# Performance work log

Hardware: AMD Instinct MI355X
Metric: run time of the kernel (lower is better)

Reference implementation:

```python
import jax, jax.numpy as jnp
import numpy as np

DIM = 224
HEADS = 8
DH = 28
WS = 8
INNER = DH * HEADS  # 224
SCALE = DH ** -0.5
B, H, W = 256, 32, 32


def setup_inputs() -> dict:
    key = jax.random.key(0)
    ks = jax.random.split(key, 6)
    x = jax.random.normal(ks[0], (B, H, W, DIM), jnp.float32)
    Wq = jax.random.normal(ks[1], (DIM, INNER), jnp.float32) * 0.02
    Wkv = jax.random.normal(ks[2], (DIM, 2 * INNER), jnp.float32) * 0.02
    Wo = jax.random.normal(ks[3], (INNER, DIM), jnp.float32) * 0.02
    bo = jnp.zeros((DIM,), jnp.float32)
    seq_l1 = WS * WS                      # 64 tokens per window
    hw = 256 // HEADS                     # 32
    seq_l2 = hw * hw // seq_l1            # 16 windows
    pos_emb1 = jax.random.normal(ks[4], (1, 1, HEADS // 2, seq_l1, seq_l1), jnp.float32)
    pos_emb2 = jax.random.normal(ks[5], (1, 1, HEADS // 2, seq_l2, seq_l2), jnp.float32)
    return {"x": x, "Wq": Wq, "Wkv": Wkv, "Wo": Wo, "bo": bo,
            "pos_emb1": pos_emb1, "pos_emb2": pos_emb2}


def _win_part(t):
    # [b, H, W, c] -> [b, n_windows, WS*WS, c]
    b, h, w, c = t.shape
    t = t.reshape(b, h // WS, WS, w // WS, WS, c).transpose(0, 1, 3, 2, 4, 5)
    return t.reshape(b, (h // WS) * (w // WS), WS * WS, c)


def _win_merge(t, h, w):
    # [b, n_windows, WS*WS, c] -> [b, H, W, c]
    b, n, mm, c = t.shape
    t = t.reshape(b, h // WS, w // WS, WS, WS, c).transpose(0, 1, 3, 2, 4, 5)
    return t.reshape(b, h, w, c)


def _attn(q, k, v, pos):
    # q,k,v: [b, n, mm, ch]; split into HEADS//2 heads of dim d
    b, n, mm, ch = q.shape
    hh = HEADS // 2
    d = ch // hh
    def sp(t):
        return t.reshape(b, n, mm, hh, d).transpose(0, 1, 3, 2, 4)  # [b,n,hh,mm,d]
    q, k, v = sp(q) * SCALE, sp(k), sp(v)
    sim = jnp.einsum('bnhid,bnhjd->bnhij', q, k) + pos
    sim = jnp.roll(sim, (1, 1), axis=(3, 4))
    attn = jax.nn.softmax(sim, axis=-1)
    o = jnp.einsum('bnhij,bnhjd->bnhid', attn, v)
    return o.transpose(0, 1, 3, 2, 4).reshape(b, n, mm, ch)


def reference(x, Wq, Wkv, Wo, bo, pos_emb1, pos_emb2):
    b, h, w, c = x.shape
    q = x @ Wq
    kv = x @ Wkv
    k, v = kv[..., :INNER], kv[..., INNER:]
    half = c // 2
    # Branch 1: local attention within each 8x8 window (first half of channels)
    q1, k1, v1 = (_win_part(t[..., :half]) for t in (q, k, v))
    out1 = _attn(q1, k1, v1, pos_emb1)  # [b, n, mm, half]
    # Branch 2: attention across windows at same intra-window position (second half)
    q2, k2, v2 = (_win_part(t[..., half:]).transpose(0, 2, 1, 3) for t in (q, k, v))
    out2 = _attn(q2, k2, v2, pos_emb2).transpose(0, 2, 1, 3)  # [b, n, mm, half]
    out = jnp.concatenate([out1, out2], axis=-1) @ Wo + bo
    return _win_merge(out, h, w)
```

## Files before the change

### kernel.cpp

```cpp
#include <hip/hip_runtime.h>

typedef __bf16 bf16_t;
typedef __bf16 bf16x4 __attribute__((ext_vector_type(4)));
typedef __bf16 bf16x8 __attribute__((ext_vector_type(8)));
typedef float  f32x4  __attribute__((ext_vector_type(4)));

#define MFMA16(a, b, c) __builtin_amdgcn_mfma_f32_16x16x32_bf16((a), (b), (c), 0, 0, 0)

#define ATT_SCALE 0.1889822365046136f

__device__ __forceinline__ bf16x8 load8_masked(const bf16_t* p, bool full) {
  bf16x4 lo = *reinterpret_cast<const bf16x4*>(p);
  bf16x4 hi = {};
  if (full) hi = *reinterpret_cast<const bf16x4*>(p + 4);
  bf16x8 r;
  r[0] = lo[0]; r[1] = lo[1]; r[2] = lo[2]; r[3] = lo[3];
  r[4] = hi[0]; r[5] = hi[1]; r[6] = hi[2]; r[7] = hi[3];
  return r;
}

__global__ __launch_bounds__(256) void prep_w(
    const float* __restrict__ Wq, const float* __restrict__ Wkv,
    const float* __restrict__ Wo,
    bf16_t* __restrict__ wsw_qkv, bf16_t* __restrict__ wsw_o) {
  const int id = blockIdx.x * 256 + threadIdx.x;
  const int buf = id / 6272;
  const int rem = id % 6272;
  const int ks = rem / 896, rem2 = rem % 896;
  const int nt = rem2 / 64, lane = rem2 % 64;
  const int col = lane & 15, g = lane >> 4;
  const int n = nt * 16 + col;
  const int k0 = ks * 32 + g * 8;
  const float* src;
  int stride;
  if (buf == 0)      { src = Wq + n;        stride = 224; }
  else if (buf == 1) { src = Wkv + n;       stride = 448; }
  else if (buf == 2) { src = Wkv + 224 + n; stride = 448; }
  else               { src = Wo + n;        stride = 224; }
  bf16x8 o;
#pragma unroll
  for (int e = 0; e < 8; ++e) o[e] = (bf16_t)src[(size_t)(k0 + e) * stride];
  bf16_t* dst = (buf < 3) ? (wsw_qkv + buf * 100352) : wsw_o;
  *reinterpret_cast<bf16x8*>(dst + ((ks * 14 + nt) * 64 + lane) * 8) = o;
}

__global__ __launch_bounds__(256, 4) void qkv_gemm(
    const float* __restrict__ x, const bf16_t* __restrict__ wsw,
    bf16_t* __restrict__ q, bf16_t* __restrict__ k, bf16_t* __restrict__ v) {
  __shared__ bf16_t xs[64][232];
  const int tid = threadIdx.x;
  const int blk = blockIdx.x;
  const int mt = blk / 3, chunk = blk % 3;
  const int b = mt >> 4, win = mt & 15;
  for (int idx = tid; idx < 64 * 56; idx += 256) {
    const int r = idx / 56, c4 = idx % 56;
    const int hh = ((win >> 2) << 3) | (r >> 3);
    const int ww = ((win & 3) << 3) | (r & 7);
    const float4 f = *reinterpret_cast<const float4*>(
        x + (size_t)((b * 32 + hh) * 32 + ww) * 224 + c4 * 4);
    bf16x4 o;
    o[0] = (bf16_t)f.x; o[1] = (bf16_t)f.y; o[2] = (bf16_t)f.z; o[3] = (bf16_t)f.w;
    *reinterpret_cast<bf16x4*>(&xs[r][c4 * 4]) = o;
  }
  const int lane = tid & 63, wid = tid >> 6;
  const int col = lane & 15, g = lane >> 4;
  const int wr = wid >> 1, wc = wid & 1;
  const bf16_t* wt = wsw + chunk * 100352;
  bf16_t* dst = (chunk == 0) ? q : ((chunk == 1) ? k : v);
  f32x4 acc[2][7];
  const f32x4 vzero = {0.f, 0.f, 0.f, 0.f};
#pragma unroll
  for (int ti = 0; ti < 2; ++ti)
#pragma unroll
    for (int tj = 0; tj < 7; ++tj) acc[ti][tj] = vzero;
  __syncthreads();
#pragma unroll
  for (int ks = 0; ks < 7; ++ks) {
    bf16x8 af0 = *reinterpret_cast<const bf16x8*>(&xs[wr * 32 + col][ks * 32 + g * 8]);
    bf16x8 af1 = *reinterpret_cast<const bf16x8*>(&xs[wr * 32 + 16 + col][ks * 32 + g * 8]);
#pragma unroll
    for (int tj = 0; tj < 7; ++tj) {
      const bf16x8 bfr = *reinterpret_cast<const bf16x8*>(
          wt + (((ks * 14) + wc * 7 + tj) * 64 + lane) * 8);
      acc[0][tj] = MFMA16(af0, bfr, acc[0][tj]);
      acc[1][tj] = MFMA16(af1, bfr, acc[1][tj]);
    }
  }
  const size_t base = (size_t)mt * 64;
#pragma unroll
  for (int ti = 0; ti < 2; ++ti)
#pragma unroll
    for (int tj = 0; tj < 7; ++tj)
#pragma unroll
      for (int r = 0; r < 4; ++r) {
        const int row = wr * 32 + ti * 16 + g * 4 + r;
        const int cn = wc * 112 + tj * 16 + col;
        dst[(base + row) * 224 + cn] = (bf16_t)acc[ti][tj][r];
      }
}

__global__ __launch_bounds__(256) void attn1(
    const bf16_t* __restrict__ q, const bf16_t* __restrict__ k,
    const bf16_t* __restrict__ v, const float* __restrict__ pos1,
    bf16_t* __restrict__ ao) {
  __shared__ bf16_t Vt[4][32][72];
  __shared__ bf16_t Pl[4][64][72];
  const int tid = threadIdx.x, blk = blockIdx.x;
  const int wid = tid >> 6, lane = tid & 63;
  const int col = lane & 15, g = lane >> 4;
  const size_t rowbase = (size_t)blk * 64;
  {
    const bf16_t* src = v + (rowbase + lane) * 224 + 28 * wid;
    const int j = (lane + 63) & 63;
#pragma unroll
    for (int c = 0; c < 28; c += 4) {
      const bf16x4 d = *reinterpret_cast<const bf16x4*>(src + c);
      Vt[wid][c + 0][j] = d[0]; Vt[wid][c + 1][j] = d[1];
      Vt[wid][c + 2][j] = d[2]; Vt[wid][c + 3][j] = d[3];
    }
#pragma unroll
    for (int c = 28; c < 32; ++c) Vt[wid][c][lane] = (bf16_t)0.f;
  }
  bf16x8 aQ[4], bK[4];
#pragma unroll
  for (int t = 0; t < 4; ++t) {
    const size_t off = (rowbase + t * 16 + col) * 224 + 28 * wid + 8 * g;
    aQ[t] = load8_masked(q + off, g < 3);
    bK[t] = load8_masked(k + off, g < 3);
  }
  const f32x4 vzero = {0.f, 0.f, 0.f, 0.f};
  f32x4 s[4][4];
#pragma unroll
  for (int ti = 0; ti < 4; ++ti)
#pragma unroll
    for (int tj = 0; tj < 4; ++tj)
      s[ti][tj] = MFMA16(aQ[ti], bK[tj], vzero);
  const float* pe = pos1 + wid * 4096;
#pragma unroll
  for (int ti = 0; ti < 4; ++ti)
#pragma unroll
    for (int tj = 0; tj < 4; ++tj)
#pragma unroll
      for (int r = 0; r < 4; ++r)
        s[ti][tj][r] = s[ti][tj][r] * ATT_SCALE +
                       pe[(ti * 16 + g * 4 + r) * 64 + tj * 16 + col];
#pragma unroll
  for (int ti = 0; ti < 4; ++ti) {
#pragma unroll
    for (int r = 0; r < 4; ++r) {
      float m = fmaxf(fmaxf(s[ti][0][r], s[ti][1][r]), fmaxf(s[ti][2][r], s[ti][3][r]));
#pragma unroll
      for (int d = 1; d < 16; d <<= 1) m = fmaxf(m, __shfl_xor(m, d));
      float sum = 0.f;
#pragma unroll
      for (int tj = 0; tj < 4; ++tj) {
        const float e = __expf(s[ti][tj][r] - m);
        s[ti][tj][r] = e; sum += e;
      }
#pragma unroll
      for (int d = 1; d < 16; d <<= 1) sum += __shfl_xor(sum, d);
      const float inv = 1.f / sum;
#pragma unroll
      for (int tj = 0; tj < 4; ++tj) s[ti][tj][r] *= inv;
    }
  }
#pragma unroll
  for (int ti = 0; ti < 4; ++ti)
#pragma unroll
    for (int tj = 0; tj < 4; ++tj)
#pragma unroll
      for (int r = 0; r < 4; ++r)
        Pl[wid][ti * 16 + g * 4 + r][tj * 16 + col] = (bf16_t)s[ti][tj][r];
  __syncthreads();
#pragma unroll
  for (int ti = 0; ti < 4; ++ti)
#pragma unroll
    for (int t2 = 0; t2 < 2; ++t2) {
      f32x4 o = vzero;
#pragma unroll
      for (int ks = 0; ks < 2; ++ks) {
        const bf16x8 aP = *reinterpret_cast<const bf16x8*>(&Pl[wid][ti * 16 + col][ks * 32 + g * 8]);
        const bf16x8 bV = *reinterpret_cast<const bf16x8*>(&Vt[wid][t2 * 16 + col][ks * 32 + g * 8]);
        o = MFMA16(aP, bV, o);
      }
      const int ch = t2 * 16 + col;
      if (ch < 28) {
#pragma unroll
        for (int r = 0; r < 4; ++r) {
          const int i = ti * 16 + g * 4 + r;
          ao[(rowbase + ((i + 1) & 63)) * 224 + 28 * wid + ch] = (bf16_t)o[r];
        }
      }
    }
}

__global__ __launch_bounds__(256) void attn2(
    const bf16_t* __restrict__ q, const bf16_t* __restrict__ k,
    const bf16_t* __restrict__ v, const float* __restrict__ pos2,
    bf16_t* __restrict__ ao) {
  __shared__ bf16_t Vt2[4][32][40];
  __shared__ bf16_t P2[4][16][40];
  const int tid = threadIdx.x, blk = blockIdx.x;
  const int wid = tid >> 6, lane = tid & 63;
  const int col = lane & 15, g = lane >> 4;
  const int b = blk >> 4;
  const int pos = (blk & 15) * 4 + wid;
  {
    unsigned short* z1 = reinterpret_cast<unsigned short*>(&Vt2[wid][0][0]);
    for (int i = lane; i < 32 * 40; i += 64) z1[i] = 0;
    unsigned short* z2 = reinterpret_cast<unsigned short*>(&P2[wid][0][0]);
    for (int i = lane; i < 16 * 40; i += 64) z2[i] = 0;
  }
  __syncthreads();
  const f32x4 vzero = {0.f, 0.f, 0.f, 0.f};
  for (int h = 0; h < 4; ++h) {
    {
      const bf16_t* src = v + ((size_t)(b * 16 + col) * 64 + pos) * 224 + 112 + 28 * h + 7 * g;
      const int jd = (col + 15) & 15;
#pragma unroll
      for (int i = 0; i < 7; ++i) Vt2[wid][7 * g + i][jd] = src[i];
    }
    const size_t off = ((size_t)(b * 16 + col) * 64 + pos) * 224 + 112 + 28 * h + 8 * g;
    const bf16x8 aQ = load8_masked(q + off, g < 3);
    const bf16x8 bK = load8_masked(k + off, g < 3);
    f32x4 s = MFMA16(aQ, bK, vzero);
    const float* pe = pos2 + h * 256;
#pragma unroll
    for (int r = 0; r < 4; ++r)
      s[r] = s[r] * ATT_SCALE + pe[(g * 4 + r) * 16 + col];
#pragma unroll
    for (int r = 0; r < 4; ++r) {
      float m = s[r];
#pragma unroll
      for (int d = 1; d < 16; d <<= 1) m = fmaxf(m, __shfl_xor(m, d));
      const float e = __expf(s[r] - m);
      float sum = e;
#pragma unroll
      for (int d = 1; d < 16; d <<= 1) sum += __shfl_xor(sum, d);
      s[r] = e / sum;
    }
#pragma unroll
    for (int r = 0; r < 4; ++r) P2[wid][g * 4 + r][col] = (bf16_t)s[r];
    __syncthreads();
    const bf16x8 aP = *reinterpret_cast<const bf16x8*>(&P2[wid][col][g * 8]);
#pragma unroll
    for (int t2 = 0; t2 < 2; ++t2) {
      const bf16x8 bV = *reinterpret_cast<const bf16x8*>(&Vt2[wid][t2 * 16 + col][g * 8]);
      const f32x4 o = MFMA16(aP, bV, vzero);
      const int ch = t2 * 16 + col;
      if (ch < 28) {
#pragma unroll
        for (int r = 0; r < 4; ++r) {
          const int wo = ((g * 4 + r) + 1) & 15;
          ao[((size_t)(b * 16 + wo) * 64 + pos) * 224 + 112 + 28 * h + ch] = (bf16_t)o[r];
        }
      }
    }
    __syncthreads();
  }
}

__global__ __launch_bounds__(256, 4) void out_gemm(
    const bf16_t* __restrict__ ao, const bf16_t* __restrict__ wsw,
    const float* __restrict__ bo, float* __restrict__ out) {
  __shared__ bf16_t xs[64][232];
  const int tid = threadIdx.x, blk = blockIdx.x;
  for (int idx = tid; idx < 64 * 28; idx += 256) {
    const int r = idx / 28, sg = idx % 28;
    *reinterpret_cast<uint4*>(&xs[r][sg * 8]) =
        *reinterpret_cast<const uint4*>(ao + ((size_t)blk * 64 + r) * 224 + sg * 8);
  }
  const int lane = tid & 63, wid = tid >> 6;
  const int col = lane & 15, g = lane >> 4;
  const int wr = wid >> 1, wc = wid & 1;
  f32x4 acc[2][7];
  const f32x4 vzero = {0.f, 0.f, 0.f, 0.f};
#pragma unroll
  for (int ti = 0; ti < 2; ++ti)
#pragma unroll
    for (int tj = 0; tj < 7; ++tj) acc[ti][tj] = vzero;
  __syncthreads();
#pragma unroll
  for (int ks = 0; ks < 7; ++ks) {
    bf16x8 af0 = *reinterpret_cast<const bf16x8*>(&xs[wr * 32 + col][ks * 32 + g * 8]);
    bf16x8 af1 = *reinterpret_cast<const bf16x8*>(&xs[wr * 32 + 16 + col][ks * 32 + g * 8]);
#pragma unroll
    for (int tj = 0; tj < 7; ++tj) {
      const bf16x8 bfr = *reinterpret_cast<const bf16x8*>(
          wsw + (((ks * 14) + wc * 7 + tj) * 64 + lane) * 8);
      acc[0][tj] = MFMA16(af0, bfr, acc[0][tj]);
      acc[1][tj] = MFMA16(af1, bfr, acc[1][tj]);
    }
  }
  float bias[7];
#pragma unroll
  for (int tj = 0; tj < 7; ++tj) bias[tj] = bo[wc * 112 + tj * 16 + col];
  const int b = blk >> 4, win = blk & 15;
#pragma unroll
  for (int ti = 0; ti < 2; ++ti)
#pragma unroll
    for (int tj = 0; tj < 7; ++tj)
#pragma unroll
      for (int r = 0; r < 4; ++r) {
        const int p = wr * 32 + ti * 16 + g * 4 + r;
        const int cn = wc * 112 + tj * 16 + col;
        const int hh = ((win >> 2) << 3) | (p >> 3);
        const int ww = ((win & 3) << 3) | (p & 7);
        out[(size_t)((b * 32 + hh) * 32 + ww) * 224 + cn] = acc[ti][tj][r] + bias[tj];
      }
}

extern "C" void kernel_launch(void* const* d_in, const int* in_sizes, int n_in,
                              void* d_out, int out_size, void* d_ws, size_t ws_size,
                              hipStream_t stream) {
  const float* x   = (const float*)d_in[0];
  const float* Wq  = (const float*)d_in[1];
  const float* Wkv = (const float*)d_in[2];
  const float* Wo  = (const float*)d_in[3];
  const float* bo  = (const float*)d_in[4];
  const float* p1  = (const float*)d_in[5];
  const float* p2  = (const float*)d_in[6];
  char* w = (char*)d_ws;
  bf16_t* q_ws    = (bf16_t*)(w);
  bf16_t* k_ws    = (bf16_t*)(w + 117440512);
  bf16_t* v_ws    = (bf16_t*)(w + 234881024);
  bf16_t* ao_ws   = (bf16_t*)(w + 352321536);
  bf16_t* wsw_qkv = (bf16_t*)(w + 469762048);
  bf16_t* wsw_o   = (bf16_t*)(w + 470063104);

  prep_w<<<98, 256, 0, stream>>>(Wq, Wkv, Wo, wsw_qkv, wsw_o);
  qkv_gemm<<<12288, 256, 0, stream>>>(x, wsw_qkv, q_ws, k_ws, v_ws);
  attn1<<<4096, 256, 0, stream>>>(q_ws, k_ws, v_ws, p1, ao_ws);
  attn2<<<4096, 256, 0, stream>>>(q_ws, k_ws, v_ws, p2, ao_ws);
  out_gemm<<<4096, 256, 0, stream>>>(ao_ws, wsw_o, bo, (float*)d_out);
}
```

Baseline: 1.010 ms.

## Fuse QKV chunks per block, split Q/K/V by branch with branch-2 transposed layout

Each qkv_gemm block now computes all three Q/K/V chunks from one staged x tile instead of three blocks each re-reading and converting x. It writes branch-1 and branch-2 halves into separate 112-wide buffers, with branch 2 stored window-transposed so attn2 reads contiguous rows instead of strided gathers. attn1 moves to 512 threads, splitting query rows across two wave groups per head. The cost is fewer qkv blocks with a serial chunk loop and a larger workspace.

```diff
diff --git a/kernel.cpp b/kernel.cpp
--- a/kernel.cpp
+++ b/kernel.cpp
@@ -46,11 +46,10 @@
 
 __global__ __launch_bounds__(256, 4) void qkv_gemm(
     const float* __restrict__ x, const bf16_t* __restrict__ wsw,
-    bf16_t* __restrict__ q, bf16_t* __restrict__ k, bf16_t* __restrict__ v) {
+    bf16_t* __restrict__ q1, bf16_t* __restrict__ k1, bf16_t* __restrict__ v1,
+    bf16_t* __restrict__ q2, bf16_t* __restrict__ k2, bf16_t* __restrict__ v2) {
   __shared__ bf16_t xs[64][232];
-  const int tid = threadIdx.x;
-  const int blk = blockIdx.x;
-  const int mt = blk / 3, chunk = blk % 3;
+  const int tid = threadIdx.x, mt = blockIdx.x;
   const int b = mt >> 4, win = mt & 15;
   for (int idx = tid; idx < 64 * 56; idx += 256) {
     const int r = idx / 56, c4 = idx % 56;
@@ -65,41 +64,57 @@
   const int lane = tid & 63, wid = tid >> 6;
   const int col = lane & 15, g = lane >> 4;
   const int wr = wid >> 1, wc = wid & 1;
-  const bf16_t* wt = wsw + chunk * 100352;
-  bf16_t* dst = (chunk == 0) ? q : ((chunk == 1) ? k : v);
-  f32x4 acc[2][7];
   const f32x4 vzero = {0.f, 0.f, 0.f, 0.f};
-#pragma unroll
-  for (int ti = 0; ti < 2; ++ti)
-#pragma unroll
-    for (int tj = 0; tj < 7; ++tj) acc[ti][tj] = vzero;
   __syncthreads();
-#pragma unroll
-  for (int ks = 0; ks < 7; ++ks) {
-    bf16x8 af0 = *reinterpret_cast<const bf16x8*>(&xs[wr * 32 + col][ks * 32 + g * 8]);
-    bf16x8 af1 = *reinterpret_cast<const bf16x8*>(&xs[wr * 32 + 16 + col][ks * 32 + g * 8]);
-#pragma unroll
-    for (int tj = 0; tj < 7; ++tj) {
-      const bf16x8 bfr = *reinterpret_cast<const bf16x8*>(
-          wt + (((ks * 14) + wc * 7 + tj) * 64 + lane) * 8);
-      acc[0][tj] = MFMA16(af0, bfr, acc[0][tj]);
-      acc[1][tj] = MFMA16(af1, bfr, acc[1][tj]);
-    }
-  }
-  const size_t base = (size_t)mt * 64;
-#pragma unroll
-  for (int ti = 0; ti < 2; ++ti)
-#pragma unroll
-    for (int tj = 0; tj < 7; ++tj)
-#pragma unroll
-      for (int r = 0; r < 4; ++r) {
-        const int row = wr * 32 + ti * 16 + g * 4 + r;
-        const int cn = wc * 112 + tj * 16 + col;
-        dst[(base + row) * 224 + cn] = (bf16_t)acc[ti][tj][r];
-      }
-}
-
-__global__ __launch_bounds__(256) void attn1(
+#pragma unroll 1
+  for (int chunk = 0; chunk < 3; ++chunk) {
+    const bf16_t* wt = wsw + chunk * 100352;
+    f32x4 acc[2][7];
+#pragma unroll
+    for (int ti = 0; ti < 2; ++ti)
+#pragma unroll
+      for (int tj = 0; tj < 7; ++tj) acc[ti][tj] = vzero;
+#pragma unroll
+    for (int ks = 0; ks < 7; ++ks) {
+      bf16x8 af0 = *reinterpret_cast<const bf16x8*>(&xs[wr * 32 + col][ks * 32 + g * 8]);
+      bf16x8 af1 = *reinterpret_cast<const bf16x8*>(&xs[wr * 32 + 16 + col][ks * 32 + g * 8]);
+#pragma unroll
+      for (int tj = 0; tj < 7; ++tj) {
+        const bf16x8 bfr = *reinterpret_cast<const bf16x8*>(
+            wt + (((ks * 14) + wc * 7 + tj) * 64 + lane) * 8);
+        acc[0][tj] = MFMA16(af0, bfr, acc[0][tj]);
+        acc[1][tj] = MFMA16(af1, bfr, acc[1][tj]);
+      }
+    }
+    bf16_t* d1 = (chunk == 0) ? q1 : ((chunk == 1) ? k1 : v1);
+    bf16_t* d2 = (chunk == 0) ? q2 : ((chunk == 1) ? k2 : v2);
+    if (wc == 0) {
+#pragma unroll
+      for (int ti = 0; ti < 2; ++ti)
+#pragma unroll
+        for (int tj = 0; tj < 7; ++tj)
+#pragma unroll
+          for (int r = 0; r < 4; ++r) {
+            const int row = wr * 32 + ti * 16 + g * 4 + r;
+            const int cn = tj * 16 + col;
+            d1[((size_t)mt * 64 + row) * 112 + cn] = (bf16_t)acc[ti][tj][r];
+          }
+    } else {
+#pragma unroll
+      for (int ti = 0; ti < 2; ++ti)
+#pragma unroll
+        for (int tj = 0; tj < 7; ++tj)
+#pragma unroll
+          for (int r = 0; r < 4; ++r) {
+            const int row = wr * 32 + ti * 16 + g * 4 + r;
+            const int cn = tj * 16 + col;
+            d2[(((size_t)b * 64 + row) * 16 + win) * 112 + cn] = (bf16_t)acc[ti][tj][r];
+          }
+    }
+  }
+}
+
+__global__ __launch_bounds__(512) void attn1(
     const bf16_t* __restrict__ q, const bf16_t* __restrict__ k,
     const bf16_t* __restrict__ v, const float* __restrict__ pos1,
     bf16_t* __restrict__ ao) {
@@ -107,45 +122,50 @@
   __shared__ bf16_t Pl[4][64][72];
   const int tid = threadIdx.x, blk = blockIdx.x;
   const int wid = tid >> 6, lane = tid & 63;
+  const int head = wid & 3, rh = wid >> 2;
   const int col = lane & 15, g = lane >> 4;
   const size_t rowbase = (size_t)blk * 64;
-  {
-    const bf16_t* src = v + (rowbase + lane) * 224 + 28 * wid;
+  if (rh == 0) {
+    const bf16_t* src = v + (rowbase + lane) * 112 + 28 * head;
     const int j = (lane + 63) & 63;
 #pragma unroll
     for (int c = 0; c < 28; c += 4) {
       const bf16x4 d = *reinterpret_cast<const bf16x4*>(src + c);
-      Vt[wid][c + 0][j] = d[0]; Vt[wid][c + 1][j] = d[1];
-      Vt[wid][c + 2][j] = d[2]; Vt[wid][c + 3][j] = d[3];
-    }
-#pragma unroll
-    for (int c = 28; c < 32; ++c) Vt[wid][c][lane] = (bf16_t)0.f;
-  }
-  bf16x8 aQ[4], bK[4];
+      Vt[head][c + 0][j] = d[0]; Vt[head][c + 1][j] = d[1];
+      Vt[head][c + 2][j] = d[2]; Vt[head][c + 3][j] = d[3];
+    }
+#pragma unroll
+    for (int c = 28; c < 32; ++c) Vt[head][c][lane] = (bf16_t)0.f;
+  }
+  bf16x8 aQ[2], bK[4];
+#pragma unroll
+  for (int t = 0; t < 2; ++t) {
+    const size_t off = (rowbase + (rh * 2 + t) * 16 + col) * 112 + 28 * head + 8 * g;
+    aQ[t] = load8_masked(q + off, g < 3);
+  }
 #pragma unroll
   for (int t = 0; t < 4; ++t) {
-    const size_t off = (rowbase + t * 16 + col) * 224 + 28 * wid + 8 * g;
-    aQ[t] = load8_masked(q + off, g < 3);
+    const size_t off = (rowbase + t * 16 + col) * 112 + 28 * head + 8 * g;
     bK[t] = load8_masked(k + off, g < 3);
   }
   const f32x4 vzero = {0.f, 0.f, 0.f, 0.f};
-  f32x4 s[4][4];
-#pragma unroll
-  for (int ti = 0; ti < 4; ++ti)
+  f32x4 s[2][4];
+#pragma unroll
+  for (int ti = 0; ti < 2; ++ti)
 #pragma unroll
     for (int tj = 0; tj < 4; ++tj)
       s[ti][tj] = MFMA16(aQ[ti], bK[tj], vzero);
-  const float* pe = pos1 + wid * 4096;
-#pragma unroll
-  for (int ti = 0; ti < 4; ++ti)
+  const float* pe = pos1 + head * 4096;
+#pragma unroll
+  for (int ti = 0; ti < 2; ++ti)
 #pragma unroll
     for (int tj = 0; tj < 4; ++tj)
 #pragma unroll
       for (int r = 0; r < 4; ++r)
         s[ti][tj][r] = s[ti][tj][r] * ATT_SCALE +
-                       pe[(ti * 16 + g * 4 + r) * 64 + tj * 16 + col];
-#pragma unroll
-  for (int ti = 0; ti < 4; ++ti) {
+                       pe[((rh * 2 + ti) * 16 + g * 4 + r) * 64 + tj * 16 + col];
+#pragma unroll
+  for (int ti = 0; ti < 2; ++ti) {
 #pragma unroll
     for (int r = 0; r < 4; ++r) {
       float m = fmaxf(fmaxf(s[ti][0][r], s[ti][1][r]), fmaxf(s[ti][2][r], s[ti][3][r]));
@@ -165,38 +185,40 @@
     }
   }
 #pragma unroll
-  for (int ti = 0; ti < 4; ++ti)
+  for (int ti = 0; ti < 2; ++ti)
 #pragma unroll
     for (int tj = 0; tj < 4; ++tj)
 #pragma unroll
       for (int r = 0; r < 4; ++r)
-        Pl[wid][ti * 16 + g * 4 + r][tj * 16 + col] = (bf16_t)s[ti][tj][r];
+        Pl[head][(rh * 2 + ti) * 16 + g * 4 + r][tj * 16 + col] = (bf16_t)s[ti][tj][r];
   __syncthreads();
 #pragma unroll
-  for (int ti = 0; ti < 4; ++ti)
+  for (int ti = 0; ti < 2; ++ti)
 #pragma unroll
     for (int t2 = 0; t2 < 2; ++t2) {
       f32x4 o = vzero;
 #pragma unroll
       for (int ks = 0; ks < 2; ++ks) {
-        const bf16x8 aP = *reinterpret_cast<const bf16x8*>(&Pl[wid][ti * 16 + col][ks * 32 + g * 8]);
-        const bf16x8 bV = *reinterpret_cast<const bf16x8*>(&Vt[wid][t2 * 16 + col][ks * 32 + g * 8]);
+        const bf16x8 aP = *reinterpret_cast<const bf16x8*>(
+            &Pl[head][(rh * 2 + ti) * 16 + col][ks * 32 + g * 8]);
+        const bf16x8 bV = *reinterpret_cast<const bf16x8*>(
+            &Vt[head][t2 * 16 + col][ks * 32 + g * 8]);
         o = MFMA16(aP, bV, o);
       }
       const int ch = t2 * 16 + col;
       if (ch < 28) {
 #pragma unroll
         for (int r = 0; r < 4; ++r) {
-          const int i = ti * 16 + g * 4 + r;
-          ao[(rowbase + ((i + 1) & 63)) * 224 + 28 * wid + ch] = (bf16_t)o[r];
+          const int i = (rh * 2 + ti) * 16 + g * 4 + r;
+          ao[(rowbase + ((i + 1) & 63)) * 224 + 28 * head + ch] = (bf16_t)o[r];
         }
       }
     }
 }
 
 __global__ __launch_bounds__(256) void attn2(
-    const bf16_t* __restrict__ q, const bf16_t* __restrict__ k,
-    const bf16_t* __restrict__ v, const float* __restrict__ pos2,
+    const bf16_t* __restrict__ q2, const bf16_t* __restrict__ k2,
+    const bf16_t* __restrict__ v2, const float* __restrict__ pos2,
     bf16_t* __restrict__ ao) {
   __shared__ bf16_t Vt2[4][32][40];
   __shared__ bf16_t P2[4][16][40];
@@ -205,6 +227,7 @@
   const int col = lane & 15, g = lane >> 4;
   const int b = blk >> 4;
   const int pos = (blk & 15) * 4 + wid;
+  const size_t base = ((size_t)b * 64 + pos) * 16;
   {
     unsigned short* z1 = reinterpret_cast<unsigned short*>(&Vt2[wid][0][0]);
     for (int i = lane; i < 32 * 40; i += 64) z1[i] = 0;
@@ -215,14 +238,14 @@
   const f32x4 vzero = {0.f, 0.f, 0.f, 0.f};
   for (int h = 0; h < 4; ++h) {
     {
-      const bf16_t* src = v + ((size_t)(b * 16 + col) * 64 + pos) * 224 + 112 + 28 * h + 7 * g;
+      const bf16_t* src = v2 + (base + col) * 112 + 28 * h + 7 * g;
       const int jd = (col + 15) & 15;
 #pragma unroll
       for (int i = 0; i < 7; ++i) Vt2[wid][7 * g + i][jd] = src[i];
     }
-    const size_t off = ((size_t)(b * 16 + col) * 64 + pos) * 224 + 112 + 28 * h + 8 * g;
-    const bf16x8 aQ = load8_masked(q + off, g < 3);
-    const bf16x8 bK = load8_masked(k + off, g < 3);
+    const size_t off = (base + col) * 112 + 28 * h + 8 * g;
+    const bf16x8 aQ = load8_masked(q2 + off, g < 3);
+    const bf16x8 bK = load8_masked(k2 + off, g < 3);
     f32x4 s = MFMA16(aQ, bK, vzero);
     const float* pe = pos2 + h * 256;
 #pragma unroll
@@ -321,16 +344,21 @@
   const float* p1  = (const float*)d_in[5];
   const float* p2  = (const float*)d_in[6];
   char* w = (char*)d_ws;
-  bf16_t* q_ws    = (bf16_t*)(w);
-  bf16_t* k_ws    = (bf16_t*)(w + 117440512);
-  bf16_t* v_ws    = (bf16_t*)(w + 234881024);
-  bf16_t* ao_ws   = (bf16_t*)(w + 352321536);
-  bf16_t* wsw_qkv = (bf16_t*)(w + 469762048);
-  bf16_t* wsw_o   = (bf16_t*)(w + 470063104);
+  const size_t HSZ = 58720256;
+  bf16_t* q1_ws   = (bf16_t*)(w);
+  bf16_t* k1_ws   = (bf16_t*)(w + HSZ);
+  bf16_t* v1_ws   = (bf16_t*)(w + 2 * HSZ);
+  bf16_t* q2_ws   = (bf16_t*)(w + 3 * HSZ);
+  bf16_t* k2_ws   = (bf16_t*)(w + 4 * HSZ);
+  bf16_t* v2_ws   = (bf16_t*)(w + 5 * HSZ);
+  bf16_t* ao_ws   = (bf16_t*)(w + 6 * HSZ);
+  bf16_t* wsw_qkv = (bf16_t*)(w + 6 * HSZ + 117440512);
+  bf16_t* wsw_o   = (bf16_t*)(w + 6 * HSZ + 117440512 + 602112);
 
   prep_w<<<98, 256, 0, stream>>>(Wq, Wkv, Wo, wsw_qkv, wsw_o);
-  qkv_gemm<<<12288, 256, 0, stream>>>(x, wsw_qkv, q_ws, k_ws, v_ws);
-  attn1<<<4096, 256, 0, stream>>>(q_ws, k_ws, v_ws, p1, ao_ws);
-  attn2<<<4096, 256, 0, stream>>>(q_ws, k_ws, v_ws, p2, ao_ws);
+  qkv_gemm<<<4096, 256, 0, stream>>>(x, wsw_qkv, q1_ws, k1_ws, v1_ws,
+                                     q2_ws, k2_ws, v2_ws);
+  attn1<<<4096, 512, 0, stream>>>(q1_ws, k1_ws, v1_ws, p1, ao_ws);
+  attn2<<<4096, 256, 0, stream>>>(q2_ws, k2_ws, v2_ws, p2, ao_ws);
   out_gemm<<<4096, 256, 0, stream>>>(ao_ws, wsw_o, bo, (float*)d_out);
 }
```

New measurement: 1.029 ms. No clear change (+1.9%).
